# Kernel tuning notes

Hardware: AMD Instinct MI355X
Metric: run time of the kernel (lower is better)

## Reference

```python
import jax, jax.numpy as jnp
import numpy as np

N = 50000
E = 500000
H = 128


def setup_inputs() -> dict:
    key = jax.random.key(0)
    ks = jax.random.split(key, 7)
    x = jax.random.normal(ks[0], (N, 4, H), dtype=jnp.float32)
    edge_index = jax.random.randint(ks[1], (2, E), 0, N, dtype=jnp.int64)
    s = 1.0 / np.sqrt(H)
    W_s_rel = jax.random.normal(ks[2], (H, H), dtype=jnp.float32) * s
    W_s_root = jax.random.normal(ks[3], (H, H), dtype=jnp.float32) * s
    b_s_root = jax.random.normal(ks[4], (H,), dtype=jnp.float32) * s
    W_v_rel = jax.random.normal(ks[5], (H, H), dtype=jnp.float32) * s
    W_v_root = jax.random.normal(ks[6], (H, H), dtype=jnp.float32) * s
    return {"x": x, "edge_index": edge_index, "W_s_rel": W_s_rel,
            "W_s_root": W_s_root, "b_s_root": b_s_root,
            "W_v_rel": W_v_rel, "W_v_root": W_v_root}


def reference(x, edge_index, W_s_rel, W_s_root, b_s_root, W_v_rel, W_v_root):
    # x: (N, 4, H); channel 0 is scalar, channels 1:4 are a 3-vector per feature
    scalar = x[:, 0, :]          # (N, H)
    vector = x[:, 1:, :]         # (N, 3, H)
    row, col = edge_index[0], edge_index[1]
    n = scalar.shape[0]

    # Per-edge messages: gather source (col) features, project with rel weights
    scalar_msg = scalar[col] @ W_s_rel.T                     # (E, H)
    vector_msg = jnp.einsum('evh,oh->evo', vector[col], W_v_rel)  # (E, 3, H)

    # Scatter-add into destination (row) nodes
    scalar_agg = jax.ops.segment_sum(scalar_msg, row, num_segments=n)
    vector_agg = jax.ops.segment_sum(vector_msg, row, num_segments=n)

    scalar_out = scalar @ W_s_root.T + b_s_root + scalar_agg          # (N, H)
    vector_out = jnp.einsum('nvh,oh->nvo', vector, W_v_root) + vector_agg  # (N, 3, H)

    return jnp.concatenate([scalar_out[:, None, :], vector_out], axis=1)  # (N, 4, H)
```

## Files before the change

kernel.cpp:

```cpp
#include <hip/hip_runtime.h>


typedef short bfrag __attribute__((ext_vector_type(8)));
typedef float cfrag __attribute__((ext_vector_type(16)));

__device__ __forceinline__ short f2bf(float f) {
    unsigned u = __builtin_bit_cast(unsigned, f);
    u += 0x7fff + ((u >> 16) & 1);
    return (short)(u >> 16);
}
__device__ __forceinline__ float bf2f(short s) {
    unsigned u = ((unsigned)(unsigned short)s) << 16;
    return __builtin_bit_cast(float, u);
}
__device__ __forceinline__ bfrag pack8(float4 lo, float4 hi) {
    bfrag r;
    r[0] = f2bf(lo.x); r[1] = f2bf(lo.y); r[2] = f2bf(lo.z); r[3] = f2bf(lo.w);
    r[4] = f2bf(hi.x); r[5] = f2bf(hi.y); r[6] = f2bf(hi.z); r[7] = f2bf(hi.w);
    return r;
}

__global__ __launch_bounds__(256) void hist_kernel(
    const int* __restrict__ ei, int* __restrict__ counts, int E)
{
    int e = blockIdx.x * 256 + threadIdx.x;
    if (e < E) atomicAdd(&counts[ei[e]], 1);
}

__global__ __launch_bounds__(1024) void scan_local_kernel(
    const int* __restrict__ counts, int* __restrict__ offsets,
    int* __restrict__ blocksums, int N)
{
    __shared__ int wsum[16];
    const int tid = threadIdx.x, lane = tid & 63, wid = tid >> 6;
    int i = blockIdx.x * 1024 + tid;
    int v = (i < N) ? counts[i] : 0;
    int incl = v;
    #pragma unroll
    for (int off = 1; off < 64; off <<= 1) {
        int t = __shfl_up(incl, off, 64);
        if (lane >= off) incl += t;
    }
    if (lane == 63) wsum[wid] = incl;
    __syncthreads();
    if (wid == 0) {
        int ws = (lane < 16) ? wsum[lane] : 0;
        int wincl = ws;
        #pragma unroll
        for (int off = 1; off < 16; off <<= 1) {
            int t = __shfl_up(wincl, off, 64);
            if (lane >= off) wincl += t;
        }
        if (lane < 16) wsum[lane] = wincl - ws;
    }
    __syncthreads();
    int excl = incl - v + wsum[wid];
    if (i < N) offsets[i] = excl;
    if (tid == 1023) blocksums[blockIdx.x] = excl + v;
}

__global__ __launch_bounds__(64) void scan_blocksums_kernel(
    int* __restrict__ bs, int nb)
{
    int lane = threadIdx.x;
    int v = (lane < nb) ? bs[lane] : 0;
    int incl = v;
    #pragma unroll
    for (int off = 1; off < 64; off <<= 1) {
        int t = __shfl_up(incl, off, 64);
        if (lane >= off) incl += t;
    }
    if (lane < nb) bs[lane] = incl - v;
}

__global__ __launch_bounds__(1024) void scan_add_kernel(
    int* __restrict__ offsets, int* __restrict__ cursor,
    const int* __restrict__ bs, int N, int E)
{
    int i = blockIdx.x * 1024 + threadIdx.x;
    if (i < N) {
        int v = offsets[i] + bs[blockIdx.x];
        offsets[i] = v;
        cursor[i] = v;
    }
    if (i == 0) offsets[N] = E;
}

__global__ __launch_bounds__(256) void bin_kernel(
    const int* __restrict__ ei, int* __restrict__ cursor,
    int* __restrict__ bins, int E)
{
    int e = blockIdx.x * 256 + threadIdx.x;
    if (e < E) {
        int row = ei[e], col = ei[E + e];
        int pos = atomicAdd(&cursor[row], 1);
        bins[pos] = col;
    }
}

__global__ __launch_bounds__(256) void conv_x_kernel(
    const float* __restrict__ x, short* __restrict__ xbf, long long total8)
{
    long long i = (long long)blockIdx.x * 256 + threadIdx.x;
    if (i >= total8) return;
    float4 lo = *(const float4*)(x + i * 8);
    float4 hi = *(const float4*)(x + i * 8 + 4);
    *(bfrag*)(xbf + i * 8) = pack8(lo, hi);
}

__global__ __launch_bounds__(256) void conv_w_kernel(
    const float* __restrict__ w0, const float* __restrict__ w1,
    const float* __restrict__ w2, const float* __restrict__ w3,
    short* __restrict__ wbf)
{
    int i = blockIdx.x * 256 + threadIdx.x;
    int j = i * 8;
    int m = j >> 14, off = j & 16383;
    const float* src = (m == 0) ? w0 : (m == 1) ? w1 : (m == 2) ? w2 : w3;
    float4 lo = *(const float4*)(src + off);
    float4 hi = *(const float4*)(src + off + 4);
    *(bfrag*)(wbf + j) = pack8(lo, hi);
}

template<int XBF>
__global__ __launch_bounds__(256) void aggregate_kernel(
    const float* __restrict__ x, const short* __restrict__ xbf,
    const int* __restrict__ offsets, const int* __restrict__ bins,
    float* __restrict__ out, int Nn)
{
    int n = blockIdx.x * 4 + (threadIdx.x >> 6);
    if (n >= Nn) return;
    int lane = threadIdx.x & 63;
    int beg = offsets[n], end = offsets[n + 1];
    float acc[8] = {0, 0, 0, 0, 0, 0, 0, 0};
    int e = beg;
    for (; e + 4 <= end; e += 4) {
        int c0 = bins[e], c1 = bins[e + 1], c2 = bins[e + 2], c3 = bins[e + 3];
        if (XBF) {
            bfrag v0 = *(const bfrag*)(xbf + (size_t)c0 * 512 + lane * 8);
            bfrag v1 = *(const bfrag*)(xbf + (size_t)c1 * 512 + lane * 8);
            bfrag v2 = *(const bfrag*)(xbf + (size_t)c2 * 512 + lane * 8);
            bfrag v3 = *(const bfrag*)(xbf + (size_t)c3 * 512 + lane * 8);
            #pragma unroll
            for (int j = 0; j < 8; j++)
                acc[j] += (bf2f(v0[j]) + bf2f(v1[j])) + (bf2f(v2[j]) + bf2f(v3[j]));
        } else {
            float4 l0 = *(const float4*)(x + (size_t)c0 * 512 + lane * 8);
            float4 h0 = *(const float4*)(x + (size_t)c0 * 512 + lane * 8 + 4);
            float4 l1 = *(const float4*)(x + (size_t)c1 * 512 + lane * 8);
            float4 h1 = *(const float4*)(x + (size_t)c1 * 512 + lane * 8 + 4);
            float4 l2 = *(const float4*)(x + (size_t)c2 * 512 + lane * 8);
            float4 h2 = *(const float4*)(x + (size_t)c2 * 512 + lane * 8 + 4);
            float4 l3 = *(const float4*)(x + (size_t)c3 * 512 + lane * 8);
            float4 h3 = *(const float4*)(x + (size_t)c3 * 512 + lane * 8 + 4);
            acc[0] += (l0.x + l1.x) + (l2.x + l3.x);
            acc[1] += (l0.y + l1.y) + (l2.y + l3.y);
            acc[2] += (l0.z + l1.z) + (l2.z + l3.z);
            acc[3] += (l0.w + l1.w) + (l2.w + l3.w);
            acc[4] += (h0.x + h1.x) + (h2.x + h3.x);
            acc[5] += (h0.y + h1.y) + (h2.y + h3.y);
            acc[6] += (h0.z + h1.z) + (h2.z + h3.z);
            acc[7] += (h0.w + h1.w) + (h2.w + h3.w);
        }
    }
    for (; e < end; e++) {
        int c = bins[e];
        if (XBF) {
            bfrag v = *(const bfrag*)(xbf + (size_t)c * 512 + lane * 8);
            #pragma unroll
            for (int j = 0; j < 8; j++) acc[j] += bf2f(v[j]);
        } else {
            float4 l = *(const float4*)(x + (size_t)c * 512 + lane * 8);
            float4 h = *(const float4*)(x + (size_t)c * 512 + lane * 8 + 4);
            acc[0] += l.x; acc[1] += l.y; acc[2] += l.z; acc[3] += l.w;
            acc[4] += h.x; acc[5] += h.y; acc[6] += h.z; acc[7] += h.w;
        }
    }
    float4 o0 = make_float4(acc[0], acc[1], acc[2], acc[3]);
    float4 o1 = make_float4(acc[4], acc[5], acc[6], acc[7]);
    *(float4*)(out + (size_t)n * 512 + lane * 8)     = o0;
    *(float4*)(out + (size_t)n * 512 + lane * 8 + 4) = o1;
}

template<int XBF>
__global__ __launch_bounds__(256) void transform_mfma(
    const float* __restrict__ x, const short* __restrict__ xbf,
    float* __restrict__ out, const short* __restrict__ wbf,
    const float* __restrict__ b_s, int Nn)
{
    const int tid = threadIdx.x;
    const int c = tid >> 6;
    const int lane = tid & 63;
    const int l31 = lane & 31;
    const int kg = lane >> 5;
    const int n0 = blockIdx.x * 32;
    int m = n0 + l31; if (m >= Nn) m = Nn - 1;
    const size_t arow = ((size_t)m * 4 + c) * 128;
    const short* wroot = wbf + ((c == 0) ? 0 : 2) * 16384;
    const short* wrel  = wbf + ((c == 0) ? 1 : 3) * 16384;

    cfrag acc[4];
    #pragma unroll
    for (int t = 0; t < 4; t++)
        #pragma unroll
        for (int r = 0; r < 16; r++) acc[t][r] = 0.f;

    #pragma unroll
    for (int ks = 0; ks < 8; ks++) {
        const int k0 = ks * 16 + kg * 8;
        bfrag a;
        if (XBF) {
            a = *(const bfrag*)(xbf + arow + k0);
        } else {
            float4 lo = *(const float4*)(x + arow + k0);
            float4 hi = *(const float4*)(x + arow + k0 + 4);
            a = pack8(lo, hi);
        }
        #pragma unroll
        for (int t = 0; t < 4; t++) {
            bfrag b = *(const bfrag*)(wroot + (size_t)(t * 32 + l31) * 128 + k0);
            acc[t] = __builtin_amdgcn_mfma_f32_32x32x16_bf16(a, b, acc[t], 0, 0, 0);
        }
    }
    #pragma unroll
    for (int ks = 0; ks < 8; ks++) {
        const int k0 = ks * 16 + kg * 8;
        float4 lo = *(const float4*)(out + arow + k0);
        float4 hi = *(const float4*)(out + arow + k0 + 4);
        bfrag a = pack8(lo, hi);
        #pragma unroll
        for (int t = 0; t < 4; t++) {
            bfrag b = *(const bfrag*)(wrel + (size_t)(t * 32 + l31) * 128 + k0);
            acc[t] = __builtin_amdgcn_mfma_f32_32x32x16_bf16(a, b, acc[t], 0, 0, 0);
        }
    }

    float bv[4] = {0.f, 0.f, 0.f, 0.f};
    if (c == 0) {
        #pragma unroll
        for (int t = 0; t < 4; t++) bv[t] = b_s[t * 32 + l31];
    }

    #pragma unroll
    for (int t = 0; t < 4; t++) {
        #pragma unroll
        for (int r = 0; r < 16; r++) {
            int row = (r & 3) + 8 * (r >> 2) + 4 * kg;
            int node = n0 + row;
            if (node < Nn)
                out[((size_t)node * 4 + c) * 128 + t * 32 + l31] = acc[t][r] + bv[t];
        }
    }
}

extern "C" void kernel_launch(void* const* d_in, const int* in_sizes, int n_in,
                              void* d_out, int out_size, void* d_ws, size_t ws_size,
                              hipStream_t stream) {
    const float* x        = (const float*)d_in[0];
    const int*   ei       = (const int*)d_in[1];
    const float* W_s_rel  = (const float*)d_in[2];
    const float* W_s_root = (const float*)d_in[3];
    const float* b_s_root = (const float*)d_in[4];
    const float* W_v_rel  = (const float*)d_in[5];
    const float* W_v_root = (const float*)d_in[6];
    float* out = (float*)d_out;

    int N = in_sizes[0] / 512;
    int E = in_sizes[1] / 2;

    size_t ints_bytes = ((size_t)(3 * N + 1) + E + 64) * sizeof(int);
    size_t wbf_bytes  = 65536 * sizeof(short);
    size_t xbf_bytes  = (size_t)N * 512 * sizeof(short);
    bool use_bf = (ws_size >= wbf_bytes + xbf_bytes + ints_bytes);

    short* wbf = (short*)d_ws;
    short* xbf = wbf + 65536;
    int* counts = use_bf ? (int*)(xbf + (size_t)N * 512) : (int*)xbf;
    int* offsets   = counts + N;
    int* cursor    = offsets + N + 1;
    int* bins      = cursor + N;
    int* blocksums = bins + E;

    int nb = (N + 1023) / 1024;

    hipMemsetAsync(counts, 0, (size_t)N * sizeof(int), stream);
    hist_kernel<<<(E + 255) / 256, 256, 0, stream>>>(ei, counts, E);
    scan_local_kernel<<<nb, 1024, 0, stream>>>(counts, offsets, blocksums, N);
    scan_blocksums_kernel<<<1, 64, 0, stream>>>(blocksums, nb);
    scan_add_kernel<<<nb, 1024, 0, stream>>>(offsets, cursor, blocksums, N, E);
    bin_kernel<<<(E + 255) / 256, 256, 0, stream>>>(ei, cursor, bins, E);

    conv_w_kernel<<<32, 256, 0, stream>>>(W_s_root, W_s_rel, W_v_root, W_v_rel, wbf);

    if (use_bf) {
        long long total8 = (long long)N * 64;
        conv_x_kernel<<<(int)((total8 + 255) / 256), 256, 0, stream>>>(x, xbf, total8);
        aggregate_kernel<1><<<(N + 3) / 4, 256, 0, stream>>>(x, xbf, offsets, bins, out, N);
        transform_mfma<1><<<(N + 31) / 32, 256, 0, stream>>>(x, xbf, out, wbf, b_s_root, N);
    } else {
        aggregate_kernel<0><<<(N + 3) / 4, 256, 0, stream>>>(x, nullptr, offsets, bins, out, N);
        transform_mfma<0><<<(N + 31) / 32, 256, 0, stream>>>(x, nullptr, out, wbf, b_s_root, N);
    }
}
```

Measured before the change: 401.5 us.

## Fuse neighbor aggregation into MFMA transform via swizzled shared-memory tile

Merges the aggregation kernel and the MFMA transform kernel into one. Each block first gathers and sums neighbor features for its 32 nodes, writes them as bf16 into an XOR-swizzled LDS tile, then runs the root and rel MFMAs from registers and LDS. This removes the fp32 write and re-read of the aggregated sums through global memory and one kernel launch. The cost is fewer, larger blocks with 32KB LDS each, and the gather phase now runs serially per node within each wave, which can reduce latency hiding.

```diff
diff --git a/kernel.cpp b/kernel.cpp
--- a/kernel.cpp
+++ b/kernel.cpp
@@ -123,115 +123,117 @@
 }
 
 template<int XBF>
-__global__ __launch_bounds__(256) void aggregate_kernel(
+__global__ __launch_bounds__(256) void fused_agg_mfma(
     const float* __restrict__ x, const short* __restrict__ xbf,
     const int* __restrict__ offsets, const int* __restrict__ bins,
-    float* __restrict__ out, int Nn)
-{
-    int n = blockIdx.x * 4 + (threadIdx.x >> 6);
-    if (n >= Nn) return;
-    int lane = threadIdx.x & 63;
-    int beg = offsets[n], end = offsets[n + 1];
-    float acc[8] = {0, 0, 0, 0, 0, 0, 0, 0};
-    int e = beg;
-    for (; e + 4 <= end; e += 4) {
-        int c0 = bins[e], c1 = bins[e + 1], c2 = bins[e + 2], c3 = bins[e + 3];
-        if (XBF) {
-            bfrag v0 = *(const bfrag*)(xbf + (size_t)c0 * 512 + lane * 8);
-            bfrag v1 = *(const bfrag*)(xbf + (size_t)c1 * 512 + lane * 8);
-            bfrag v2 = *(const bfrag*)(xbf + (size_t)c2 * 512 + lane * 8);
-            bfrag v3 = *(const bfrag*)(xbf + (size_t)c3 * 512 + lane * 8);
-            #pragma unroll
-            for (int j = 0; j < 8; j++)
-                acc[j] += (bf2f(v0[j]) + bf2f(v1[j])) + (bf2f(v2[j]) + bf2f(v3[j]));
-        } else {
-            float4 l0 = *(const float4*)(x + (size_t)c0 * 512 + lane * 8);
-            float4 h0 = *(const float4*)(x + (size_t)c0 * 512 + lane * 8 + 4);
-            float4 l1 = *(const float4*)(x + (size_t)c1 * 512 + lane * 8);
-            float4 h1 = *(const float4*)(x + (size_t)c1 * 512 + lane * 8 + 4);
-            float4 l2 = *(const float4*)(x + (size_t)c2 * 512 + lane * 8);
-            float4 h2 = *(const float4*)(x + (size_t)c2 * 512 + lane * 8 + 4);
-            float4 l3 = *(const float4*)(x + (size_t)c3 * 512 + lane * 8);
-            float4 h3 = *(const float4*)(x + (size_t)c3 * 512 + lane * 8 + 4);
-            acc[0] += (l0.x + l1.x) + (l2.x + l3.x);
-            acc[1] += (l0.y + l1.y) + (l2.y + l3.y);
-            acc[2] += (l0.z + l1.z) + (l2.z + l3.z);
-            acc[3] += (l0.w + l1.w) + (l2.w + l3.w);
-            acc[4] += (h0.x + h1.x) + (h2.x + h3.x);
-            acc[5] += (h0.y + h1.y) + (h2.y + h3.y);
-            acc[6] += (h0.z + h1.z) + (h2.z + h3.z);
-            acc[7] += (h0.w + h1.w) + (h2.w + h3.w);
-        }
-    }
-    for (; e < end; e++) {
-        int c = bins[e];
-        if (XBF) {
-            bfrag v = *(const bfrag*)(xbf + (size_t)c * 512 + lane * 8);
-            #pragma unroll
-            for (int j = 0; j < 8; j++) acc[j] += bf2f(v[j]);
-        } else {
-            float4 l = *(const float4*)(x + (size_t)c * 512 + lane * 8);
-            float4 h = *(const float4*)(x + (size_t)c * 512 + lane * 8 + 4);
-            acc[0] += l.x; acc[1] += l.y; acc[2] += l.z; acc[3] += l.w;
-            acc[4] += h.x; acc[5] += h.y; acc[6] += h.z; acc[7] += h.w;
-        }
-    }
-    float4 o0 = make_float4(acc[0], acc[1], acc[2], acc[3]);
-    float4 o1 = make_float4(acc[4], acc[5], acc[6], acc[7]);
-    *(float4*)(out + (size_t)n * 512 + lane * 8)     = o0;
-    *(float4*)(out + (size_t)n * 512 + lane * 8 + 4) = o1;
-}
-
-template<int XBF>
-__global__ __launch_bounds__(256) void transform_mfma(
-    const float* __restrict__ x, const short* __restrict__ xbf,
     float* __restrict__ out, const short* __restrict__ wbf,
     const float* __restrict__ b_s, int Nn)
 {
-    const int tid = threadIdx.x;
-    const int c = tid >> 6;
+    __shared__ short atile[32 * 512];
+    const int tid  = threadIdx.x;
+    const int wid  = tid >> 6;
     const int lane = tid & 63;
+    const int n0   = blockIdx.x * 32;
+
+    const int cl   = lane >> 4;
+    const int slot = lane & 15;
+    #pragma unroll 1
+    for (int i = 0; i < 8; i++) {
+        const int m = wid * 8 + i;
+        const int n = n0 + m;
+        float acc[8] = {0, 0, 0, 0, 0, 0, 0, 0};
+        if (n < Nn) {
+            const int beg = offsets[n], end = offsets[n + 1];
+            int e = beg;
+            for (; e + 4 <= end; e += 4) {
+                int c0 = bins[e], c1 = bins[e + 1], c2 = bins[e + 2], c3 = bins[e + 3];
+                if (XBF) {
+                    bfrag v0 = *(const bfrag*)(xbf + (size_t)c0 * 512 + lane * 8);
+                    bfrag v1 = *(const bfrag*)(xbf + (size_t)c1 * 512 + lane * 8);
+                    bfrag v2 = *(const bfrag*)(xbf + (size_t)c2 * 512 + lane * 8);
+                    bfrag v3 = *(const bfrag*)(xbf + (size_t)c3 * 512 + lane * 8);
+                    #pragma unroll
+                    for (int j = 0; j < 8; j++)
+                        acc[j] += (bf2f(v0[j]) + bf2f(v1[j])) + (bf2f(v2[j]) + bf2f(v3[j]));
+                } else {
+                    float4 l0 = *(const float4*)(x + (size_t)c0 * 512 + lane * 8);
+                    float4 h0 = *(const float4*)(x + (size_t)c0 * 512 + lane * 8 + 4);
+                    float4 l1 = *(const float4*)(x + (size_t)c1 * 512 + lane * 8);
+                    float4 h1 = *(const float4*)(x + (size_t)c1 * 512 + lane * 8 + 4);
+                    float4 l2 = *(const float4*)(x + (size_t)c2 * 512 + lane * 8);
+                    float4 h2 = *(const float4*)(x + (size_t)c2 * 512 + lane * 8 + 4);
+                    float4 l3 = *(const float4*)(x + (size_t)c3 * 512 + lane * 8);
+                    float4 h3 = *(const float4*)(x + (size_t)c3 * 512 + lane * 8 + 4);
+                    acc[0] += (l0.x + l1.x) + (l2.x + l3.x);
+                    acc[1] += (l0.y + l1.y) + (l2.y + l3.y);
+                    acc[2] += (l0.z + l1.z) + (l2.z + l3.z);
+                    acc[3] += (l0.w + l1.w) + (l2.w + l3.w);
+                    acc[4] += (h0.x + h1.x) + (h2.x + h3.x);
+                    acc[5] += (h0.y + h1.y) + (h2.y + h3.y);
+                    acc[6] += (h0.z + h1.z) + (h2.z + h3.z);
+                    acc[7] += (h0.w + h1.w) + (h2.w + h3.w);
+                }
+            }
+            for (; e < end; e++) {
+                int cc = bins[e];
+                if (XBF) {
+                    bfrag v = *(const bfrag*)(xbf + (size_t)cc * 512 + lane * 8);
+                    #pragma unroll
+                    for (int j = 0; j < 8; j++) acc[j] += bf2f(v[j]);
+                } else {
+                    float4 l = *(const float4*)(x + (size_t)cc * 512 + lane * 8);
+                    float4 h = *(const float4*)(x + (size_t)cc * 512 + lane * 8 + 4);
+                    acc[0] += l.x; acc[1] += l.y; acc[2] += l.z; acc[3] += l.w;
+                    acc[4] += h.x; acc[5] += h.y; acc[6] += h.z; acc[7] += h.w;
+                }
+            }
+        }
+        const int boff = m * 1024 + cl * 256 + ((slot * 16) ^ ((m & 15) << 4));
+        *(bfrag*)((char*)atile + boff) =
+            pack8(make_float4(acc[0], acc[1], acc[2], acc[3]),
+                  make_float4(acc[4], acc[5], acc[6], acc[7]));
+    }
+
+    const int c   = wid;
     const int l31 = lane & 31;
-    const int kg = lane >> 5;
-    const int n0 = blockIdx.x * 32;
-    int m = n0 + l31; if (m >= Nn) m = Nn - 1;
-    const size_t arow = ((size_t)m * 4 + c) * 128;
-    const short* wroot = wbf + ((c == 0) ? 0 : 2) * 16384;
-    const short* wrel  = wbf + ((c == 0) ? 1 : 3) * 16384;
-
-    cfrag acc[4];
-    #pragma unroll
-    for (int t = 0; t < 4; t++)
-        #pragma unroll
-        for (int r = 0; r < 16; r++) acc[t][r] = 0.f;
-
+    const int kg  = lane >> 5;
+    int mA = n0 + l31; if (mA >= Nn) mA = Nn - 1;
+    const size_t arow = ((size_t)mA * 4 + c) * 128;
+    bfrag a0[8];
     #pragma unroll
     for (int ks = 0; ks < 8; ks++) {
         const int k0 = ks * 16 + kg * 8;
-        bfrag a;
         if (XBF) {
-            a = *(const bfrag*)(xbf + arow + k0);
+            a0[ks] = *(const bfrag*)(xbf + arow + k0);
         } else {
             float4 lo = *(const float4*)(x + arow + k0);
             float4 hi = *(const float4*)(x + arow + k0 + 4);
-            a = pack8(lo, hi);
-        }
-        #pragma unroll
-        for (int t = 0; t < 4; t++) {
-            bfrag b = *(const bfrag*)(wroot + (size_t)(t * 32 + l31) * 128 + k0);
-            acc[t] = __builtin_amdgcn_mfma_f32_32x32x16_bf16(a, b, acc[t], 0, 0, 0);
-        }
-    }
+            a0[ks] = pack8(lo, hi);
+        }
+    }
+
+    __syncthreads();
+
+    const short* wroot = wbf + ((c == 0) ? 0 : 2) * 16384;
+    const short* wrel  = wbf + ((c == 0) ? 1 : 3) * 16384;
+
+    cfrag acc4[4];
+    #pragma unroll
+    for (int t = 0; t < 4; t++)
+        #pragma unroll
+        for (int r = 0; r < 16; r++) acc4[t][r] = 0.f;
+
     #pragma unroll
     for (int ks = 0; ks < 8; ks++) {
         const int k0 = ks * 16 + kg * 8;
-        float4 lo = *(const float4*)(out + arow + k0);
-        float4 hi = *(const float4*)(out + arow + k0 + 4);
-        bfrag a = pack8(lo, hi);
+        const int rboff = l31 * 1024 + c * 256 + ((k0 * 2) ^ ((l31 & 15) << 4));
+        bfrag a1 = *(const bfrag*)((const char*)atile + rboff);
         #pragma unroll
         for (int t = 0; t < 4; t++) {
-            bfrag b = *(const bfrag*)(wrel + (size_t)(t * 32 + l31) * 128 + k0);
-            acc[t] = __builtin_amdgcn_mfma_f32_32x32x16_bf16(a, b, acc[t], 0, 0, 0);
+            bfrag b0 = *(const bfrag*)(wroot + (size_t)(t * 32 + l31) * 128 + k0);
+            acc4[t] = __builtin_amdgcn_mfma_f32_32x32x16_bf16(a0[ks], b0, acc4[t], 0, 0, 0);
+            bfrag b1 = *(const bfrag*)(wrel + (size_t)(t * 32 + l31) * 128 + k0);
+            acc4[t] = __builtin_amdgcn_mfma_f32_32x32x16_bf16(a1, b1, acc4[t], 0, 0, 0);
         }
     }
 
@@ -248,7 +250,7 @@
             int row = (r & 3) + 8 * (r >> 2) + 4 * kg;
             int node = n0 + row;
             if (node < Nn)
-                out[((size_t)node * 4 + c) * 128 + t * 32 + l31] = acc[t][r] + bv[t];
+                out[((size_t)node * 4 + c) * 128 + t * 32 + l31] = acc4[t][r] + bv[t];
         }
     }
 }
@@ -295,10 +297,10 @@
     if (use_bf) {
         long long total8 = (long long)N * 64;
         conv_x_kernel<<<(int)((total8 + 255) / 256), 256, 0, stream>>>(x, xbf, total8);
-        aggregate_kernel<1><<<(N + 3) / 4, 256, 0, stream>>>(x, xbf, offsets, bins, out, N);
-        transform_mfma<1><<<(N + 31) / 32, 256, 0, stream>>>(x, xbf, out, wbf, b_s_root, N);
+        fused_agg_mfma<1><<<(N + 31) / 32, 256, 0, stream>>>(
+            x, xbf, offsets, bins, out, wbf, b_s_root, N);
     } else {
-        aggregate_kernel<0><<<(N + 3) / 4, 256, 0, stream>>>(x, nullptr, offsets, bins, out, N);
-        transform_mfma<0><<<(N + 31) / 32, 256, 0, stream>>>(x, nullptr, out, wbf, b_s_root, N);
-    }
-}
+        fused_agg_mfma<0><<<(N + 31) / 32, 256, 0, stream>>>(
+            x, nullptr, offsets, bins, out, wbf, b_s_root, N);
+    }
+}
```

After: 390.0 us. -2.9%, faster.
